# Performance work log

Hardware: AMD Instinct MI355X
Metric: run time of the kernel (lower is better)

Reference implementation:

```python
import jax, jax.numpy as jnp
import numpy as np

EPS = 1e-6
B_PAIRS, N_PER_GRAPH, D_IN, D_OUT = 128, 64, 128, 128
N_NODES = B_PAIRS * N_PER_GRAPH          # 8192 nodes on each side
N_EDGES = B_PAIRS * N_PER_GRAPH * N_PER_GRAPH  # 524288 dense bipartite edges


def setup_inputs() -> dict:
    key = jax.random.key(0)
    k1, k2, k3 = jax.random.split(key, 3)
    x_src = jax.random.normal(k1, (N_NODES, D_IN), dtype=jnp.float32)
    x_tgt = jax.random.normal(k2, (N_NODES, D_IN), dtype=jnp.float32)
    # xavier-uniform-like weight [out_nhid, in_nhid]
    bound = np.sqrt(6.0 / (D_OUT + D_IN))
    weight = jax.random.uniform(k3, (D_OUT, D_IN), dtype=jnp.float32,
                                minval=-bound, maxval=bound)
    # block-diagonal dense bipartite edges: graph pair p connects its n x n nodes
    base = np.arange(B_PAIRS, dtype=np.int64)[:, None, None] * N_PER_GRAPH
    src = (base + np.arange(N_PER_GRAPH, dtype=np.int64)[:, None]).repeat(N_PER_GRAPH, axis=2)
    dst = (base + np.arange(N_PER_GRAPH, dtype=np.int64)[None, None, :]).repeat(N_PER_GRAPH, axis=1)
    edge_src = jnp.asarray(src.reshape(-1))
    edge_dst = jnp.asarray(dst.reshape(-1))
    return {"x_src": x_src, "x_tgt": x_tgt, "weight": weight,
            "edge_src": edge_src, "edge_dst": edge_dst}


def reference(x_src, x_tgt, weight, edge_src, edge_dst):
    M = x_tgt.shape[0]
    # --- message: per-edge relu(cosine similarity), softmax-like normalization per target ---
    x_j = x_src[edge_src]                      # [E, D] gather source features
    x_i = x_tgt[edge_dst]                      # [E, D] gather target features
    n_i = jnp.linalg.norm(x_i, axis=-1, keepdims=True)
    n_j = jnp.linalg.norm(x_j, axis=-1, keepdims=True)
    x_norm = jnp.maximum(n_i * n_j, EPS)
    coef = jax.nn.relu(jnp.sum(x_i * x_j, axis=1, keepdims=True) / x_norm)  # [E,1]
    coef_sum = jax.ops.segment_sum(coef + EPS, edge_dst, num_segments=M)    # [M,1]
    norm_coef = coef / coef_sum[edge_dst]
    global_x = jax.ops.segment_sum(norm_coef * x_j, edge_dst, num_segments=M)  # [M,D]
    # --- per-output-channel cosine between weight-scaled target and aggregated features ---
    # numerator[m,o] = sum_d x_tgt[m,d] * global_x[m,d] * weight[o,d]^2  (avoids [M,O,D] blowup)
    W2 = weight * weight                       # [O, D]
    numerator = (x_tgt * global_x) @ W2.T      # [M, O]
    den_t = jnp.sqrt((x_tgt * x_tgt) @ W2.T + EPS)
    den_g = jnp.sqrt((global_x * global_x) @ W2.T + EPS)
    denominator = jnp.maximum(den_t * den_g, EPS)
    return numerator / denominator             # [M, out_nhid]
```

## Files before the change

kernel.cpp:

```cpp
#include <hip/hip_runtime.h>

#define EPS 1e-6f

typedef __bf16 bf16_t;
typedef bf16_t bf16x8 __attribute__((ext_vector_type(8)));
typedef float  f32x4  __attribute__((ext_vector_type(4)));

namespace {
constexpr int D  = 128;
constexpr int OD = 128;
constexpr int SXS_S = 136;
constexpr int SW2_S = 136;
constexpr int SCF_S = 72;
constexpr int SF_S  = 132;
}

__device__ inline bf16x8 to_bf16x8(float4 a, float4 b) {
    bf16x8 r;
    r[0] = (bf16_t)a.x; r[1] = (bf16_t)a.y; r[2] = (bf16_t)a.z; r[3] = (bf16_t)a.w;
    r[4] = (bf16_t)b.x; r[5] = (bf16_t)b.y; r[6] = (bf16_t)b.z; r[7] = (bf16_t)b.w;
    return r;
}

__global__ __launch_bounds__(256, 2)
void h2mn_fused(const float* __restrict__ x_src,
                const float* __restrict__ x_tgt,
                const float* __restrict__ weight,
                float* __restrict__ out)
{
    __shared__ __attribute__((aligned(16))) bf16_t sXs[64][SXS_S];
    __shared__ __attribute__((aligned(16))) bf16_t sW2[128][SW2_S];
    __shared__ __attribute__((aligned(16))) bf16_t sCf[16][SCF_S];
    __shared__ __attribute__((aligned(16))) float  sXt[16][SF_S];
    __shared__ __attribute__((aligned(16))) float  sGx[16][SF_S];
    __shared__ float ns[64], ntg[16], csum[16];

    const int t = threadIdx.x;
    const int p = blockIdx.x >> 2;
    const int h = blockIdx.x & 3;

    {
        const float4* src = reinterpret_cast<const float4*>(x_src + (size_t)p * 64 * D);
        #pragma unroll
        for (int k = 0; k < 4; ++k) {
            const int c = t + 256 * k;
            const int j = c >> 4, d0 = (c & 15) * 8;
            const float4 v0 = src[c * 2], v1 = src[c * 2 + 1];
            float ss = v0.x*v0.x + v0.y*v0.y + v0.z*v0.z + v0.w*v0.w
                     + v1.x*v1.x + v1.y*v1.y + v1.z*v1.z + v1.w*v1.w;
            #pragma unroll
            for (int mk = 1; mk < 16; mk <<= 1) ss += __shfl_xor(ss, mk);
            if ((t & 15) == 0) ns[j] = sqrtf(ss);
            *reinterpret_cast<bf16x8*>(&sXs[j][d0]) = to_bf16x8(v0, v1);
        }
    }
    {
        const float4* tg = reinterpret_cast<const float4*>(x_tgt + (size_t)(p * 64 + h * 16) * D);
        const int c = t;
        const int i = c >> 4, d0 = (c & 15) * 8;
        const float4 v0 = tg[c * 2], v1 = tg[c * 2 + 1];
        float ss = v0.x*v0.x + v0.y*v0.y + v0.z*v0.z + v0.w*v0.w
                 + v1.x*v1.x + v1.y*v1.y + v1.z*v1.z + v1.w*v1.w;
        #pragma unroll
        for (int mk = 1; mk < 16; mk <<= 1) ss += __shfl_xor(ss, mk);
        if ((t & 15) == 0) ntg[i] = sqrtf(ss);
        *reinterpret_cast<float4*>(&sXt[i][d0])     = v0;
        *reinterpret_cast<float4*>(&sXt[i][d0 + 4]) = v1;
    }
    {
        const float4* wv = reinterpret_cast<const float4*>(weight);
        #pragma unroll
        for (int k = 0; k < 8; ++k) {
            const int c = t + 256 * k;
            const int o = c >> 4, d0 = (c & 15) * 8;
            float4 w0 = wv[c * 2], w1 = wv[c * 2 + 1];
            w0.x *= w0.x; w0.y *= w0.y; w0.z *= w0.z; w0.w *= w0.w;
            w1.x *= w1.x; w1.y *= w1.y; w1.z *= w1.z; w1.w *= w1.w;
            *reinterpret_cast<bf16x8*>(&sW2[o][d0]) = to_bf16x8(w0, w1);
        }
    }
    __syncthreads();

    const int w  = t >> 6;
    const int ln = t & 63;
    const int mm = ln & 15;
    const int g  = ln >> 4;

    {
        const int nt = w;
        f32x4 accS = {0.f, 0.f, 0.f, 0.f};
        #pragma unroll
        for (int ks = 0; ks < 4; ++ks) {
            const float* xp = &sXt[mm][ks * 32 + g * 8];
            const float4 x0 = *reinterpret_cast<const float4*>(xp);
            const float4 x1 = *reinterpret_cast<const float4*>(xp + 4);
            const bf16x8 a = to_bf16x8(x0, x1);
            const bf16x8 b = *reinterpret_cast<const bf16x8*>(&sXs[nt * 16 + mm][ks * 32 + g * 8]);
            accS = __builtin_amdgcn_mfma_f32_16x16x32_bf16(a, b, accS, 0, 0, 0);
        }
        const int j_loc = nt * 16 + mm;
        const float nsj = ns[j_loc];
        #pragma unroll
        for (int r = 0; r < 4; ++r) {
            const int m_loc = g * 4 + r;
            const float den = fmaxf(ntg[m_loc] * nsj, EPS);
            const float cf  = fmaxf(accS[r] / den, 0.f);
            sCf[m_loc][j_loc] = (bf16_t)cf;
        }
    }
    __syncthreads();

    {
        const int row = t >> 4, c0 = (t & 15) * 4;
        float s = (float)sCf[row][c0]     + (float)sCf[row][c0 + 1]
                + (float)sCf[row][c0 + 2] + (float)sCf[row][c0 + 3];
        #pragma unroll
        for (int mk = 1; mk < 16; mk <<= 1) s += __shfl_xor(s, mk);
        if ((t & 15) == 0) csum[row] = s + 64.f * EPS;
    }
    __syncthreads();

    {
        f32x4 accG[2] = {{0.f,0.f,0.f,0.f}, {0.f,0.f,0.f,0.f}};
        #pragma unroll
        for (int ks = 0; ks < 2; ++ks) {
            const bf16x8 a = *reinterpret_cast<const bf16x8*>(&sCf[mm][ks * 32 + g * 8]);
            #pragma unroll
            for (int u = 0; u < 2; ++u) {
                const int dt = w * 2 + u;
                bf16x8 b;
                #pragma unroll
                for (int i2 = 0; i2 < 8; ++i2)
                    b[i2] = sXs[ks * 32 + g * 8 + i2][dt * 16 + mm];
                accG[u] = __builtin_amdgcn_mfma_f32_16x16x32_bf16(a, b, accG[u], 0, 0, 0);
            }
        }
        float inv[4];
        #pragma unroll
        for (int r = 0; r < 4; ++r) inv[r] = 1.f / csum[g * 4 + r];
        #pragma unroll
        for (int u = 0; u < 2; ++u) {
            const int dcol = (w * 2 + u) * 16 + mm;
            #pragma unroll
            for (int r = 0; r < 4; ++r)
                sGx[g * 4 + r][dcol] = accG[u][r] * inv[r];
        }
    }
    __syncthreads();

    {
        f32x4 nume[2] = {{0.f,0.f,0.f,0.f}, {0.f,0.f,0.f,0.f}};
        f32x4 det [2] = {{0.f,0.f,0.f,0.f}, {0.f,0.f,0.f,0.f}};
        f32x4 deg [2] = {{0.f,0.f,0.f,0.f}, {0.f,0.f,0.f,0.f}};
        #pragma unroll
        for (int ks = 0; ks < 4; ++ks) {
            const float* xp = &sXt[mm][ks * 32 + g * 8];
            const float* gp = &sGx[mm][ks * 32 + g * 8];
            const float4 x0 = *reinterpret_cast<const float4*>(xp);
            const float4 x1 = *reinterpret_cast<const float4*>(xp + 4);
            const float4 g0 = *reinterpret_cast<const float4*>(gp);
            const float4 g1 = *reinterpret_cast<const float4*>(gp + 4);
            const float xv[8] = {x0.x,x0.y,x0.z,x0.w,x1.x,x1.y,x1.z,x1.w};
            const float gv[8] = {g0.x,g0.y,g0.z,g0.w,g1.x,g1.y,g1.z,g1.w};
            bf16x8 af, bf_, cf_;
            #pragma unroll
            for (int i2 = 0; i2 < 8; ++i2) {
                af [i2] = (bf16_t)(xv[i2] * gv[i2]);
                bf_[i2] = (bf16_t)(xv[i2] * xv[i2]);
                cf_[i2] = (bf16_t)(gv[i2] * gv[i2]);
            }
            #pragma unroll
            for (int u = 0; u < 2; ++u) {
                const int ot = w * 2 + u;
                const bf16x8 wv = *reinterpret_cast<const bf16x8*>(&sW2[ot * 16 + mm][ks * 32 + g * 8]);
                nume[u] = __builtin_amdgcn_mfma_f32_16x16x32_bf16(af,  wv, nume[u], 0, 0, 0);
                det [u] = __builtin_amdgcn_mfma_f32_16x16x32_bf16(bf_, wv, det [u], 0, 0, 0);
                deg [u] = __builtin_amdgcn_mfma_f32_16x16x32_bf16(cf_, wv, deg [u], 0, 0, 0);
            }
        }
        #pragma unroll
        for (int u = 0; u < 2; ++u) {
            const int o = (w * 2 + u) * 16 + mm;
            #pragma unroll
            for (int r = 0; r < 4; ++r) {
                const int m_loc = g * 4 + r;
                const int mg = p * 64 + h * 16 + m_loc;
                const float dd = fmaxf(sqrtf(det[u][r] + EPS) * sqrtf(deg[u][r] + EPS), EPS);
                out[(size_t)mg * OD + o] = nume[u][r] / dd;
            }
        }
    }
}

extern "C" void kernel_launch(void* const* d_in, const int* in_sizes, int n_in,
                              void* d_out, int out_size, void* d_ws, size_t ws_size,
                              hipStream_t stream)
{
    const float* x_src  = (const float*)d_in[0];
    const float* x_tgt  = (const float*)d_in[1];
    const float* weight = (const float*)d_in[2];
    float* out = (float*)d_out;

    h2mn_fused<<<dim3(512), dim3(256), 0, stream>>>(x_src, x_tgt, weight, out);
}
```

Baseline: 74.61 us.

## Drop shared W2 staging, load weight rows into registers, use 512-thread blocks

Removes the shared-memory copy of the squared weight matrix. Each wave now loads its own 16 weight rows directly from global memory into registers and squares and converts them just before the MFMA. Blocks grow to 8 waves, so each wave owns one 16-column output tile instead of two; some phases run on only half the threads. This cuts LDS use (about 34KB per block) and the full weight staging pass, aiming for higher occupancy. The cost is redundant weight reads from global and L2, and idle waves in the similarity and sum phases.

```diff
diff --git a/kernel.cpp b/kernel.cpp
--- a/kernel.cpp
+++ b/kernel.cpp
@@ -10,7 +10,6 @@
 constexpr int D  = 128;
 constexpr int OD = 128;
 constexpr int SXS_S = 136;
-constexpr int SW2_S = 136;
 constexpr int SCF_S = 72;
 constexpr int SF_S  = 132;
 }
@@ -22,14 +21,13 @@
     return r;
 }
 
-__global__ __launch_bounds__(256, 2)
+__global__ __launch_bounds__(512, 4)
 void h2mn_fused(const float* __restrict__ x_src,
                 const float* __restrict__ x_tgt,
                 const float* __restrict__ weight,
                 float* __restrict__ out)
 {
     __shared__ __attribute__((aligned(16))) bf16_t sXs[64][SXS_S];
-    __shared__ __attribute__((aligned(16))) bf16_t sW2[128][SW2_S];
     __shared__ __attribute__((aligned(16))) bf16_t sCf[16][SCF_S];
     __shared__ __attribute__((aligned(16))) float  sXt[16][SF_S];
     __shared__ __attribute__((aligned(16))) float  sGx[16][SF_S];
@@ -42,8 +40,8 @@
     {
         const float4* src = reinterpret_cast<const float4*>(x_src + (size_t)p * 64 * D);
         #pragma unroll
-        for (int k = 0; k < 4; ++k) {
-            const int c = t + 256 * k;
+        for (int k = 0; k < 2; ++k) {
+            const int c = t + 512 * k;
             const int j = c >> 4, d0 = (c & 15) * 8;
             const float4 v0 = src[c * 2], v1 = src[c * 2 + 1];
             float ss = v0.x*v0.x + v0.y*v0.y + v0.z*v0.z + v0.w*v0.w
@@ -54,7 +52,7 @@
             *reinterpret_cast<bf16x8*>(&sXs[j][d0]) = to_bf16x8(v0, v1);
         }
     }
-    {
+    if (t < 256) {
         const float4* tg = reinterpret_cast<const float4*>(x_tgt + (size_t)(p * 64 + h * 16) * D);
         const int c = t;
         const int i = c >> 4, d0 = (c & 15) * 8;
@@ -67,18 +65,6 @@
         *reinterpret_cast<float4*>(&sXt[i][d0])     = v0;
         *reinterpret_cast<float4*>(&sXt[i][d0 + 4]) = v1;
     }
-    {
-        const float4* wv = reinterpret_cast<const float4*>(weight);
-        #pragma unroll
-        for (int k = 0; k < 8; ++k) {
-            const int c = t + 256 * k;
-            const int o = c >> 4, d0 = (c & 15) * 8;
-            float4 w0 = wv[c * 2], w1 = wv[c * 2 + 1];
-            w0.x *= w0.x; w0.y *= w0.y; w0.z *= w0.z; w0.w *= w0.w;
-            w1.x *= w1.x; w1.y *= w1.y; w1.z *= w1.z; w1.w *= w1.w;
-            *reinterpret_cast<bf16x8*>(&sW2[o][d0]) = to_bf16x8(w0, w1);
-        }
-    }
     __syncthreads();
 
     const int w  = t >> 6;
@@ -86,7 +72,7 @@
     const int mm = ln & 15;
     const int g  = ln >> 4;
 
-    {
+    if (w < 4) {
         const int nt = w;
         f32x4 accS = {0.f, 0.f, 0.f, 0.f};
         #pragma unroll
@@ -110,7 +96,7 @@
     }
     __syncthreads();
 
-    {
+    if (t < 256) {
         const int row = t >> 4, c0 = (t & 15) * 4;
         float s = (float)sCf[row][c0]     + (float)sCf[row][c0 + 1]
                 + (float)sCf[row][c0 + 2] + (float)sCf[row][c0 + 3];
@@ -120,38 +106,38 @@
     }
     __syncthreads();
 
+    const float* wrow = weight + (size_t)(w * 16 + mm) * D + g * 8;
+    float4 wr0[4], wr1[4];
+    #pragma unroll
+    for (int ks = 0; ks < 4; ++ks) {
+        wr0[ks] = *reinterpret_cast<const float4*>(wrow + ks * 32);
+        wr1[ks] = *reinterpret_cast<const float4*>(wrow + ks * 32 + 4);
+    }
+
     {
-        f32x4 accG[2] = {{0.f,0.f,0.f,0.f}, {0.f,0.f,0.f,0.f}};
+        f32x4 accG = {0.f, 0.f, 0.f, 0.f};
         #pragma unroll
         for (int ks = 0; ks < 2; ++ks) {
             const bf16x8 a = *reinterpret_cast<const bf16x8*>(&sCf[mm][ks * 32 + g * 8]);
+            bf16x8 b;
             #pragma unroll
-            for (int u = 0; u < 2; ++u) {
-                const int dt = w * 2 + u;
-                bf16x8 b;
-                #pragma unroll
-                for (int i2 = 0; i2 < 8; ++i2)
-                    b[i2] = sXs[ks * 32 + g * 8 + i2][dt * 16 + mm];
-                accG[u] = __builtin_amdgcn_mfma_f32_16x16x32_bf16(a, b, accG[u], 0, 0, 0);
-            }
+            for (int i2 = 0; i2 < 8; ++i2)
+                b[i2] = sXs[ks * 32 + g * 8 + i2][w * 16 + mm];
+            accG = __builtin_amdgcn_mfma_f32_16x16x32_bf16(a, b, accG, 0, 0, 0);
         }
         float inv[4];
         #pragma unroll
         for (int r = 0; r < 4; ++r) inv[r] = 1.f / csum[g * 4 + r];
         #pragma unroll
-        for (int u = 0; u < 2; ++u) {
-            const int dcol = (w * 2 + u) * 16 + mm;
-            #pragma unroll
-            for (int r = 0; r < 4; ++r)
-                sGx[g * 4 + r][dcol] = accG[u][r] * inv[r];
-        }
+        for (int r = 0; r < 4; ++r)
+            sGx[g * 4 + r][w * 16 + mm] = accG[r] * inv[r];
     }
     __syncthreads();
 
     {
-        f32x4 nume[2] = {{0.f,0.f,0.f,0.f}, {0.f,0.f,0.f,0.f}};
-        f32x4 det [2] = {{0.f,0.f,0.f,0.f}, {0.f,0.f,0.f,0.f}};
-        f32x4 deg [2] = {{0.f,0.f,0.f,0.f}, {0.f,0.f,0.f,0.f}};
+        f32x4 nume = {0.f,0.f,0.f,0.f};
+        f32x4 det  = {0.f,0.f,0.f,0.f};
+        f32x4 deg  = {0.f,0.f,0.f,0.f};
         #pragma unroll
         for (int ks = 0; ks < 4; ++ks) {
             const float* xp = &sXt[mm][ks * 32 + g * 8];
@@ -169,25 +155,21 @@
                 bf_[i2] = (bf16_t)(xv[i2] * xv[i2]);
                 cf_[i2] = (bf16_t)(gv[i2] * gv[i2]);
             }
-            #pragma unroll
-            for (int u = 0; u < 2; ++u) {
-                const int ot = w * 2 + u;
-                const bf16x8 wv = *reinterpret_cast<const bf16x8*>(&sW2[ot * 16 + mm][ks * 32 + g * 8]);
-                nume[u] = __builtin_amdgcn_mfma_f32_16x16x32_bf16(af,  wv, nume[u], 0, 0, 0);
-                det [u] = __builtin_amdgcn_mfma_f32_16x16x32_bf16(bf_, wv, det [u], 0, 0, 0);
-                deg [u] = __builtin_amdgcn_mfma_f32_16x16x32_bf16(cf_, wv, deg [u], 0, 0, 0);
-            }
+            float4 w0 = wr0[ks], w1 = wr1[ks];
+            w0.x *= w0.x; w0.y *= w0.y; w0.z *= w0.z; w0.w *= w0.w;
+            w1.x *= w1.x; w1.y *= w1.y; w1.z *= w1.z; w1.w *= w1.w;
+            const bf16x8 wv = to_bf16x8(w0, w1);
+            nume = __builtin_amdgcn_mfma_f32_16x16x32_bf16(af,  wv, nume, 0, 0, 0);
+            det  = __builtin_amdgcn_mfma_f32_16x16x32_bf16(bf_, wv, det,  0, 0, 0);
+            deg  = __builtin_amdgcn_mfma_f32_16x16x32_bf16(cf_, wv, deg,  0, 0, 0);
         }
+        const int o = w * 16 + mm;
         #pragma unroll
-        for (int u = 0; u < 2; ++u) {
-            const int o = (w * 2 + u) * 16 + mm;
-            #pragma unroll
-            for (int r = 0; r < 4; ++r) {
-                const int m_loc = g * 4 + r;
-                const int mg = p * 64 + h * 16 + m_loc;
-                const float dd = fmaxf(sqrtf(det[u][r] + EPS) * sqrtf(deg[u][r] + EPS), EPS);
-                out[(size_t)mg * OD + o] = nume[u][r] / dd;
-            }
+        for (int r = 0; r < 4; ++r) {
+            const int m_loc = g * 4 + r;
+            const int mg = p * 64 + h * 16 + m_loc;
+            const float dd = fmaxf(sqrtf(det[r] + EPS) * sqrtf(deg[r] + EPS), EPS);
+            out[(size_t)mg * OD + o] = nume[r] / dd;
         }
     }
 }
@@ -201,5 +183,5 @@
     const float* weight = (const float*)d_in[2];
     float* out = (float*)d_out;
 
-    h2mn_fused<<<dim3(512), dim3(256), 0, stream>>>(x_src, x_tgt, weight, out);
+    h2mn_fused<<<dim3(512), dim3(512), 0, stream>>>(x_src, x_tgt, weight, out);
 }
```

Measured after the change: 73.91 us. No clear change (-0.9%).
